# Kernel optimization log

Measured on AMD Instinct MI355X. Metric: run time of the kernel, lower is better.

Reference implementation:

```python
import jax, jax.numpy as jnp
import numpy as np

B, N, C, H, FF = 8, 1024, 256, 8, 4
HD = C // H

def _lin(key, din, dout):
    kw, kb = jax.random.split(key)
    lim = 1.0 / np.sqrt(din)
    W = jax.random.uniform(kw, (din, dout), minval=-lim, maxval=lim, dtype=jnp.float32)
    b = jax.random.uniform(kb, (dout,), minval=-lim, maxval=lim, dtype=jnp.float32)
    return W, b

def setup_inputs():
    key = jax.random.key(0)
    k = jax.random.split(key, 8)
    h = jax.random.normal(k[0], (B, N, C), dtype=jnp.float32)
    coords = jax.random.normal(k[1], (B, N, 3), dtype=jnp.float32) * 3.0
    mask = jnp.broadcast_to(jnp.arange(N) < int(0.9 * N), (B, N))
    Wq, bq = _lin(k[2], C, C)
    Wk, bk = _lin(k[3], C, C)
    Wv, bv = _lin(k[4], C, C)
    Wo, bo = _lin(k[5], C, C)
    Wf1, bf1 = _lin(k[6], C, FF * C)
    Wf2, bf2 = _lin(k[7], FF * C, C)
    g1 = jnp.ones((C,), jnp.float32); b1 = jnp.zeros((C,), jnp.float32)
    g2 = jnp.ones((C,), jnp.float32); b2 = jnp.zeros((C,), jnp.float32)
    return dict(h=h, coords=coords, mask=mask, Wq=Wq, bq=bq, Wk=Wk, bk=bk,
                Wv=Wv, bv=bv, Wo=Wo, bo=bo, g1=g1, b1=b1, g2=g2, b2=b2,
                Wf1=Wf1, bf1=bf1, Wf2=Wf2, bf2=bf2)

def _layernorm(x, g, b, eps=1e-5):
    mu = x.mean(-1, keepdims=True)
    var = ((x - mu) ** 2).mean(-1, keepdims=True)
    return (x - mu) / jnp.sqrt(var + eps) * g + b

def _forward(h, coords, mask, Wq, bq, Wk, bk, Wv, bv, Wo, bo,
             g1, b1, g2, b2, Wf1, bf1, Wf2, bf2):
    B_, N_, C_ = h.shape
    scale = HD ** (-0.5)
    eps = 1e-8
    # pairwise squared distance, +inf for pairs touching a masked node
    pair_mask = mask[:, :, None] & mask[:, None, :]          # [B,N,N]
    diff = coords[:, :, None, :] - coords[:, None, :, :]      # [B,N,N,3]
    r2 = jnp.where(pair_mask, (diff * diff).sum(-1), jnp.inf)
    eye = jnp.eye(N_, dtype=bool)[None]                       # [1,N,N]
    valid = jnp.isfinite(r2)
    off = valid & ~eye
    r2_off = jnp.where(off, r2, 0.0)
    cnt_row = jnp.maximum(off.sum(-1, keepdims=True), 1)
    r2_row_mean = jnp.maximum(r2_off.sum(-1, keepdims=True) / cnt_row, 1e-4)
    r2_eff = jnp.where(eye, r2_row_mean, r2)
    r2_eff = jnp.clip(jnp.nan_to_num(r2_eff, posinf=1e8), 1e-6, 1e8)
    w_raw = jnp.where(valid, 1.0 / (r2_eff + eps), 0.0)
    w = w_raw / jnp.maximum(w_raw.sum(-1, keepdims=True), 1e-12)
    log_w = jnp.log(jnp.maximum(w, 1e-12))[:, None]           # [B,1,N,N]
    # attention
    x = _layernorm(h, g1, b1)
    q = (x @ Wq + bq).reshape(B_, N_, H, HD).transpose(0, 2, 1, 3)
    k = (x @ Wk + bk).reshape(B_, N_, H, HD).transpose(0, 2, 1, 3)
    v = (x @ Wv + bv).reshape(B_, N_, H, HD).transpose(0, 2, 1, 3)
    logits = jnp.einsum('bhnd,bhmd->bhnm', q, k) * scale + log_w
    mask_q = mask[:, None, :, None]
    mask_k = mask[:, None, None, :]
    pair_valid = valid[:, None] & mask_q & mask_k
    logits = jnp.where(pair_valid, logits, -1e9)
    logits = jnp.where(mask_q, logits, 0.0)
    attn = jax.nn.softmax(logits, axis=-1)
    attn = jnp.nan_to_num(attn, nan=0.0)
    out = jnp.einsum('bhnm,bhmd->bhnd', attn, v)
    out = out * mask_q.astype(out.dtype)
    out = out.transpose(0, 2, 1, 3).reshape(B_, N_, C_)
    out = out @ Wo + bo
    h = h + out
    y = _layernorm(h, g2, b2)
    y = jax.nn.gelu(y @ Wf1 + bf1, approximate=False) @ Wf2 + bf2
    return h + y

def reference(h, coords, mask, Wq, bq, Wk, bk, Wv, bv, Wo, bo,
              g1, b1, g2, b2, Wf1, bf1, Wf2, bf2):
    return _forward(h, coords, mask, Wq, bq, Wk, bk, Wv, bv, Wo, bo,
                    g1, b1, g2, b2, Wf1, bf1, Wf2, bf2)
```

## Files before the change

### kernel.cpp

```cpp
#include <hip/hip_runtime.h>
#include <math.h>

#define NN 1024
#define CC 256
#define HH 8
#define HDD 32
#define NV 921
#define WJ 960

typedef __bf16 bf16x8 __attribute__((ext_vector_type(8)));
typedef float f32x4 __attribute__((ext_vector_type(4)));
typedef float f32x16 __attribute__((ext_vector_type(16)));
typedef unsigned short u16x4 __attribute__((ext_vector_type(4)));
typedef unsigned short u16x8 __attribute__((ext_vector_type(8)));
typedef unsigned int u32x4 __attribute__((ext_vector_type(4)));

static __device__ __forceinline__ unsigned short f2b(float x) {
  union { __bf16 h; unsigned short u; } c; c.h = (__bf16)x; return c.u;
}
static __device__ __forceinline__ float b2f(unsigned short u) {
  union { float f; unsigned v; } c; c.v = ((unsigned)u) << 16; return c.f;
}

static __device__ __forceinline__ unsigned cvt_pk_bf16(float lo, float hi) {
  unsigned r;
  asm("v_cvt_pk_bf16_f32 %0, %1, %2" : "=v"(r) : "v"(lo), "v"(hi));
  return r;
}

static __device__ __forceinline__ float block_sum(float val, float* red) {
  #pragma unroll
  for (int off = 32; off > 0; off >>= 1) val += __shfl_xor(val, off);
  __syncthreads();
  if ((threadIdx.x & 63) == 0) red[threadIdx.x >> 6] = val;
  __syncthreads();
  return red[0] + red[1] + red[2] + red[3];
}

__global__ __launch_bounds__(256) void prep_kernel(
    const float* __restrict__ coords, unsigned short* __restrict__ wP,
    const float* __restrict__ Wq, const float* __restrict__ Wk, const float* __restrict__ Wv,
    const float* __restrict__ Wo, const float* __restrict__ Wf1, const float* __restrict__ Wf2,
    unsigned short* __restrict__ qkvT, unsigned short* __restrict__ woT,
    unsigned short* __restrict__ wf1T, unsigned short* __restrict__ wf2T,
    const float* __restrict__ bq, const float* __restrict__ bk, const float* __restrict__ bv,
    float* __restrict__ bqkv,
    const float* __restrict__ h, const float* __restrict__ g1, const float* __restrict__ b1,
    unsigned short* __restrict__ x1b)
{
  __shared__ float smem[NN * 3 + 4];
  int bid = blockIdx.x;
  int tid = threadIdx.x;

  if (bid < 8192) {
    float* csh = smem;
    float* red = smem + NN * 3;
    int row = bid;
    int b = row >> 10, i = row & (NN - 1);
    unsigned short* wrow = wP + (size_t)row * WJ;
    if (i >= NV) {
      if (tid < 240) {
        ushort4 z = {0, 0, 0, 0};
        *(ushort4*)(wrow + tid * 4) = z;
      }
      return;
    }
    const float* cb = coords + (size_t)b * NN * 3;
    for (int t = tid; t < NN * 3; t += 256) csh[t] = cb[t];
    __syncthreads();
    float cix = csh[i*3+0], ciy = csh[i*3+1], ciz = csh[i*3+2];
    float r2loc[4];
    float part = 0.f;
    #pragma unroll
    for (int it = 0; it < 4; it++) {
      int j = tid + it * 256;
      float dx = cix - csh[j*3+0], dy = ciy - csh[j*3+1], dz = ciz - csh[j*3+2];
      float r2 = dx*dx + dy*dy + dz*dz;
      r2loc[it] = r2;
      if (j < NV && j != i) part += r2;
    }
    float s = block_sum(part, red);
    float rm = fmaxf(s * (1.0f / 920.0f), 1e-4f);
    float wpart = 0.f;
    #pragma unroll
    for (int it = 0; it < 4; it++) {
      int j = tid + it * 256;
      if (j < NV) {
        float r2e = (j == i) ? rm : r2loc[it];
        float r2c = fminf(fmaxf(r2e, 1e-6f), 1e8f);
        wpart += 1.0f / (r2c + 1e-8f);
      }
    }
    float sw = block_sum(wpart, red);
    float invsw = 1.0f / fmaxf(sw, 1e-12f);
    if (tid < 240) {
      ushort4 o;
      unsigned short* op = (unsigned short*)&o;
      #pragma unroll
      for (int e = 0; e < 4; e++) {
        int j = tid * 4 + e;
        float wv = 0.f;
        if (j < NV) {
          float dx = cix - csh[j*3+0], dy = ciy - csh[j*3+1], dz = ciz - csh[j*3+2];
          float r2 = dx*dx + dy*dy + dz*dz;
          float r2e = (j == i) ? rm : r2;
          float r2c = fminf(fmaxf(r2e, 1e-6f), 1e8f);
          wv = fmaxf((1.0f / (r2c + 1e-8f)) * invsw, 1e-12f);
        }
        op[e] = f2b(wv);
      }
      *(ushort4*)(wrow + tid * 4) = o;
    }
  } else if (bid < 8961) {
    int t = bid - 8192;
    if (t == 768) {
      bqkv[tid] = bq[tid]; bqkv[256 + tid] = bk[tid]; bqkv[512 + tid] = bv[tid];
      return;
    }
    float (*lds)[33] = (float(*)[33])smem;
    const float* src; unsigned short* dst; int Kd, Nd, tk, tn;
    if (t < 256) {
      int wid = t >> 6, lt = t & 63;
      const float* srcs[4] = {Wq, Wk, Wv, Wo};
      unsigned short* dsts[4] = {qkvT, qkvT + 256 * 256, qkvT + 512 * 256, woT};
      src = srcs[wid]; dst = dsts[wid]; Kd = 256; Nd = 256; tk = lt >> 3; tn = lt & 7;
    } else if (t < 512) {
      int lt = t - 256;
      src = Wf1; dst = wf1T; Kd = 256; Nd = 1024; tk = lt >> 5; tn = lt & 31;
    } else {
      int lt = t - 512;
      src = Wf2; dst = wf2T; Kd = 1024; Nd = 256; tk = lt >> 3; tn = lt & 7;
    }
    int tx = tid & 31, ty = tid >> 5;
    #pragma unroll
    for (int it = 0; it < 4; it++) {
      int r = ty + it * 8;
      lds[r][tx] = src[(size_t)(tk * 32 + r) * Nd + tn * 32 + tx];
    }
    __syncthreads();
    #pragma unroll
    for (int it = 0; it < 4; it++) {
      int r = ty + it * 8;
      dst[(size_t)(tn * 32 + r) * Kd + tk * 32 + tx] = f2b(lds[tx][r]);
    }
  } else {
    int w = tid >> 6, lane = tid & 63;
    int row = (bid - 8961) * 4 + w;
    float4 x = *(const float4*)(h + (size_t)row * CC + lane * 4);
    float s = x.x + x.y + x.z + x.w;
    #pragma unroll
    for (int off = 1; off < 64; off <<= 1) s += __shfl_xor(s, off);
    float mu = s * (1.0f / 256.0f);
    float dx0 = x.x - mu, dx1 = x.y - mu, dx2 = x.z - mu, dx3 = x.w - mu;
    float s2 = dx0*dx0 + dx1*dx1 + dx2*dx2 + dx3*dx3;
    #pragma unroll
    for (int off = 1; off < 64; off <<= 1) s2 += __shfl_xor(s2, off);
    float rstd = 1.0f / sqrtf(s2 * (1.0f / 256.0f) + 1e-5f);
    float4 gv = *(const float4*)(g1 + lane * 4);
    float4 bv2 = *(const float4*)(b1 + lane * 4);
    ushort4 o;
    o.x = f2b(dx0 * rstd * gv.x + bv2.x);
    o.y = f2b(dx1 * rstd * gv.y + bv2.y);
    o.z = f2b(dx2 * rstd * gv.z + bv2.z);
    o.w = f2b(dx3 * rstd * gv.w + bv2.w);
    *(ushort4*)(x1b + (size_t)row * CC + lane * 4) = o;
  }
}

__global__ __launch_bounds__(256) void ln_bf16_kernel(
    const float* __restrict__ X, const float* __restrict__ g, const float* __restrict__ b,
    unsigned short* __restrict__ out)
{
  int w = threadIdx.x >> 6, lane = threadIdx.x & 63;
  int row = blockIdx.x * 4 + w;
  float4 x = *(const float4*)(X + (size_t)row * CC + lane * 4);
  float s = x.x + x.y + x.z + x.w;
  #pragma unroll
  for (int off = 1; off < 64; off <<= 1) s += __shfl_xor(s, off);
  float mu = s * (1.0f / 256.0f);
  float dx0 = x.x - mu, dx1 = x.y - mu, dx2 = x.z - mu, dx3 = x.w - mu;
  float s2 = dx0*dx0 + dx1*dx1 + dx2*dx2 + dx3*dx3;
  #pragma unroll
  for (int off = 1; off < 64; off <<= 1) s2 += __shfl_xor(s2, off);
  float rstd = 1.0f / sqrtf(s2 * (1.0f / 256.0f) + 1e-5f);
  float4 gv = *(const float4*)(g + lane * 4);
  float4 bv = *(const float4*)(b + lane * 4);
  ushort4 o;
  o.x = f2b(dx0 * rstd * gv.x + bv.x);
  o.y = f2b(dx1 * rstd * gv.y + bv.y);
  o.z = f2b(dx2 * rstd * gv.z + bv.z);
  o.w = f2b(dx3 * rstd * gv.w + bv.w);
  *(ushort4*)(out + (size_t)row * CC + lane * 4) = o;
}

template<bool GELU_EP, bool RES_ADD, int OUT_MODE>
__global__ __launch_bounds__(256) void gemm_mfma_kernel(
    const unsigned short* __restrict__ A, const unsigned short* __restrict__ BT,
    const float* __restrict__ bias, const float* __restrict__ res,
    void* __restrict__ out, float oscale, int M, int N, int K)
{
  __shared__ unsigned short As[128][72];
  __shared__ unsigned short Bs[64][72];
  int tid = threadIdx.x;
  int w = tid >> 6, lane = tid & 63, lo = lane & 15, hi = lane >> 4;
  int wr = w >> 1, wc = w & 1;
  int bm = blockIdx.y * 128, bn = blockIdx.x * 64;
  f32x4 acc[4][2];
  #pragma unroll
  for (int a = 0; a < 4; a++)
    #pragma unroll
    for (int nf = 0; nf < 2; nf++) acc[a][nf] = (f32x4){0.f, 0.f, 0.f, 0.f};
  int arow = tid >> 3, acol = (tid & 7) * 8;
  u16x8 areg[4], breg[2];
  #pragma unroll
  for (int it = 0; it < 4; it++)
    areg[it] = *(const u16x8*)(A + (size_t)(bm + arow + it * 32) * K + acol);
  #pragma unroll
  for (int it = 0; it < 2; it++)
    breg[it] = *(const u16x8*)(BT + (size_t)(bn + arow + it * 32) * K + acol);
  for (int k0 = 0; k0 < K; k0 += 64) {
    __syncthreads();
    #pragma unroll
    for (int it = 0; it < 4; it++) *(u16x8*)&As[arow + it * 32][acol] = areg[it];
    #pragma unroll
    for (int it = 0; it < 2; it++) *(u16x8*)&Bs[arow + it * 32][acol] = breg[it];
    __syncthreads();
    if (k0 + 64 < K) {
      #pragma unroll
      for (int it = 0; it < 4; it++)
        areg[it] = *(const u16x8*)(A + (size_t)(bm + arow + it * 32) * K + k0 + 64 + acol);
      #pragma unroll
      for (int it = 0; it < 2; it++)
        breg[it] = *(const u16x8*)(BT + (size_t)(bn + arow + it * 32) * K + k0 + 64 + acol);
    }
    #pragma unroll
    for (int ks = 0; ks < 2; ks++) {
      bf16x8 bf0 = *(const bf16x8*)&Bs[wc * 32 + lo][ks * 32 + hi * 8];
      bf16x8 bf1 = *(const bf16x8*)&Bs[wc * 32 + 16 + lo][ks * 32 + hi * 8];
      #pragma unroll
      for (int a = 0; a < 4; a++) {
        bf16x8 af = *(const bf16x8*)&As[wr * 64 + a * 16 + lo][ks * 32 + hi * 8];
        acc[a][0] = __builtin_amdgcn_mfma_f32_16x16x32_bf16(af, bf0, acc[a][0], 0, 0, 0);
        acc[a][1] = __builtin_amdgcn_mfma_f32_16x16x32_bf16(af, bf1, acc[a][1], 0, 0, 0);
      }
    }
  }
  float bias0 = bias[bn + wc * 32 + lo];
  float bias1 = bias[bn + wc * 32 + 16 + lo];
  #pragma unroll
  for (int a = 0; a < 4; a++) {
    int gm0 = bm + wr * 64 + a * 16 + hi * 4;
    #pragma unroll
    for (int nf = 0; nf < 2; nf++) {
      int gn = bn + wc * 32 + nf * 16 + lo;
      float bb = nf ? bias1 : bias0;
      float vv[4];
      #pragma unroll
      for (int r = 0; r < 4; r++) {
        float v = acc[a][nf][r] + bb;
        if constexpr (RES_ADD) v += res[(size_t)(gm0 + r) * N + gn];
        if constexpr (GELU_EP) v = 0.5f * v * (1.0f + erff(v * 0.70710678118654752f));
        vv[r] = v;
      }
      if constexpr (OUT_MODE == 0) {
        float* of = (float*)out;
        #pragma unroll
        for (int r = 0; r < 4; r++) of[(size_t)(gm0 + r) * N + gn] = vv[r] * oscale;
      } else if constexpr (OUT_MODE == 1) {
        unsigned short* ob = (unsigned short*)out;
        #pragma unroll
        for (int r = 0; r < 4; r++) ob[(size_t)(gm0 + r) * N + gn] = f2b(vv[r] * oscale);
      } else {
        int cb = gn >> 8;
        int nl = gn & 255;
        unsigned short* qp = (unsigned short*)out;
        if (cb == 0) {
          #pragma unroll
          for (int r = 0; r < 4; r++) qp[(size_t)(gm0 + r) * 256 + nl] = f2b(vv[r] * oscale);
        } else if (cb == 1) {
          unsigned short* kp = qp + (size_t)M * 256;
          #pragma unroll
          for (int r = 0; r < 4; r++) kp[(size_t)(gm0 + r) * 256 + nl] = f2b(vv[r]);
        } else {
          unsigned short* vp = qp + (size_t)M * 512;
          int bidx = gm0 >> 10, tok = gm0 & 1023;
          ushort4 pk;
          pk.x = f2b(vv[0]); pk.y = f2b(vv[1]); pk.z = f2b(vv[2]); pk.w = f2b(vv[3]);
          *(ushort4*)&vp[(((size_t)(bidx * 256 + nl)) << 10) + tok] = pk;
        }
      }
    }
  }
}

__global__ __launch_bounds__(256, 2) void attn_mfma_kernel(
    const __bf16* __restrict__ q, const __bf16* __restrict__ k, const __bf16* __restrict__ vt,
    const unsigned short* __restrict__ wP, unsigned short* __restrict__ ao)
{
  __shared__ unsigned short Ktu[64][136];
  __shared__ unsigned short VTs[128][72];
  __shared__ unsigned short Wls[32][68];

  int tid = threadIdx.x;
  int w = tid >> 6;
  int lane = tid & 63;
  int il = lane & 31, hf = lane >> 5;
  int b = blockIdx.z, hg = blockIdx.y, it = blockIdx.x;
  int i0 = it * 32;
  int head = hg * 4 + w;
  int ig = i0 + il;

  const __bf16* qrow = q + ((size_t)(b * NN + ig)) * CC + head * HDD;
  bf16x8 qf0 = *(const bf16x8*)(qrow + hf * 8);
  bf16x8 qf1 = *(const bf16x8*)(qrow + 16 + hf * 8);

  f32x16 osum;
  #pragma unroll
  for (int r = 0; r < 16; r++) osum[r] = 0.f;
  float den = 0.f;

  int sjr = tid >> 4, scpos = (tid & 15) * 8;
  int vrow = tid >> 1, vcol = (tid & 1) * 32;
  int wrow = tid >> 3, wcol = (tid & 7) * 8;

  u16x8 kreg[4], vreg[4], wreg;

  if (i0 < NV) {
    {
      const __bf16* ksrc = k + ((size_t)(b * NN + sjr)) * CC + hg * 128 + scpos;
      #pragma unroll
      for (int rr = 0; rr < 4; rr++)
        kreg[rr] = *(const u16x8*)(ksrc + (size_t)(rr * 16) * CC);
      const __bf16* vsrc = vt + ((size_t)(b * CC + hg * 128 + vrow)) * NN + vcol;
      #pragma unroll
      for (int qq = 0; qq < 4; qq++)
        vreg[qq] = *(const u16x8*)(vsrc + qq * 8);
      wreg = *(const u16x8*)(wP + ((size_t)(b * NN + i0 + wrow)) * WJ + wcol);
    }
    for (int jt = 0; jt < 15; jt++) {
      __syncthreads();
      #pragma unroll
      for (int rr = 0; rr < 4; rr++)
        *(u16x8*)&Ktu[sjr + rr * 16][scpos] = kreg[rr];
      #pragma unroll
      for (int qq = 0; qq < 4; qq++)
        *(u16x8*)&VTs[vrow][vcol + qq * 8] = vreg[qq];
      *(u16x8*)&Wls[wrow][wcol] = wreg;
      __syncthreads();
      if (jt < 14) {
        int j0 = (jt + 1) * 64;
        const __bf16* ksrc = k + ((size_t)(b * NN + j0 + sjr)) * CC + hg * 128 + scpos;
        #pragma unroll
        for (int rr = 0; rr < 4; rr++)
          kreg[rr] = *(const u16x8*)(ksrc + (size_t)(rr * 16) * CC);
        const __bf16* vsrc = vt + ((size_t)(b * CC + hg * 128 + vrow)) * NN + j0 + vcol;
        #pragma unroll
        for (int qq = 0; qq < 4; qq++)
          vreg[qq] = *(const u16x8*)(vsrc + qq * 8);
        wreg = *(const u16x8*)(wP + ((size_t)(b * NN + i0 + wrow)) * WJ + j0 + wcol);
      }

      #pragma unroll
      for (int jblk = 0; jblk < 2; jblk++) {
        f32x16 s;
        #pragma unroll
        for (int r = 0; r < 16; r++) s[r] = 0.f;
        bf16x8 kf0 = *(const bf16x8*)&Ktu[jblk * 32 + il][w * 32 + hf * 8];
        bf16x8 kf1 = *(const bf16x8*)&Ktu[jblk * 32 + il][w * 32 + 16 + hf * 8];
        s = __builtin_amdgcn_mfma_f32_32x32x16_bf16(kf0, qf0, s, 0, 0, 0);
        s = __builtin_amdgcn_mfma_f32_32x32x16_bf16(kf1, qf1, s, 0, 0, 0);
        float p[16];
        #pragma unroll
        for (int qd = 0; qd < 4; qd++) {
          u16x4 w4 = *(const u16x4*)&Wls[il][jblk * 32 + qd * 8 + hf * 4];
          #pragma unroll
          for (int e = 0; e < 4; e++) {
            int r = qd * 4 + e;
            float pv = b2f(w4[e]) * __expf(s[r]);
            den += pv;
            p[r] = pv;
          }
        }
        #pragma unroll
        for (int kw = 0; kw < 2; kw++) {
          unsigned pk0 = cvt_pk_bf16(p[8 * kw + 0], p[8 * kw + 1]);
          unsigned pk1 = cvt_pk_bf16(p[8 * kw + 2], p[8 * kw + 3]);
          unsigned pk2 = cvt_pk_bf16(p[8 * kw + 4], p[8 * kw + 5]);
          unsigned pk3 = cvt_pk_bf16(p[8 * kw + 6], p[8 * kw + 7]);
          u32x4 frag;
#if __has_builtin(__builtin_amdgcn_permlane32_swap)
          {
            typedef unsigned uint2v __attribute__((ext_vector_type(2)));
            uint2v s02 = __builtin_amdgcn_permlane32_swap(pk0, pk2, false, false);
            uint2v s13 = __builtin_amdgcn_permlane32_swap(pk1, pk3, false, false);
            frag[0] = s02[0]; frag[1] = s13[0]; frag[2] = s02[1]; frag[3] = s13[1];
          }
#else
          {
            unsigned t0 = __shfl_xor((int)pk2, 32);
            unsigned t1 = __shfl_xor((int)pk3, 32);
            unsigned t2 = __shfl_xor((int)pk0, 32);
            unsigned t3 = __shfl_xor((int)pk1, 32);
            frag[0] = hf ? t0 : pk0;
            frag[1] = hf ? t1 : pk1;
            frag[2] = hf ? pk2 : t2;
            frag[3] = hf ? pk3 : t3;
          }
#endif
          bf16x8 pfrag;
          { union { u32x4 u; bf16x8 b; } cvt; cvt.u = frag; pfrag = cvt.b; }
          bf16x8 vfrag = *(const bf16x8*)&VTs[w * 32 + il][(jblk * 2 + kw) * 16 + hf * 8];
          osum = __builtin_amdgcn_mfma_f32_32x32x16_bf16(pfrag, vfrag, osum, 0, 0, 0);
        }
      }
    }
  }

  den += __shfl_xor(den, 32);
  float inv = (den > 0.f) ? 1.0f / den : 0.f;

  #pragma unroll
  for (int r = 0; r < 16; r++) {
    int ir = (r & 3) + 8 * (r >> 2) + 4 * hf;
    float sc = __shfl(inv, ir);
    ao[((size_t)(b * NN + i0 + ir)) * CC + head * HDD + il] = f2b(osum[r] * sc);
  }
}

extern "C" void kernel_launch(void* const* d_in, const int* in_sizes, int n_in,
                              void* d_out, int out_size, void* d_ws, size_t ws_size,
                              hipStream_t stream) {
  (void)in_sizes; (void)n_in; (void)out_size; (void)ws_size;
  const float* h      = (const float*)d_in[0];
  const float* coords = (const float*)d_in[1];
  const float* Wq  = (const float*)d_in[3];
  const float* bq  = (const float*)d_in[4];
  const float* Wk  = (const float*)d_in[5];
  const float* bk  = (const float*)d_in[6];
  const float* Wv  = (const float*)d_in[7];
  const float* bv  = (const float*)d_in[8];
  const float* Wo  = (const float*)d_in[9];
  const float* bo  = (const float*)d_in[10];
  const float* g1  = (const float*)d_in[11];
  const float* b1  = (const float*)d_in[12];
  const float* g2  = (const float*)d_in[13];
  const float* b2  = (const float*)d_in[14];
  const float* Wf1 = (const float*)d_in[15];
  const float* bf1 = (const float*)d_in[16];
  const float* Wf2 = (const float*)d_in[17];
  const float* bf2 = (const float*)d_in[18];

  const int M = 8 * NN;
  char* cur = (char*)d_ws;
  auto alloc = [&](size_t bytes) { char* p = cur; cur += (bytes + 255) & ~(size_t)255; return p; };
  unsigned short* wPb  = (unsigned short*)alloc((size_t)M * WJ * 2);
  unsigned short* qkvT = (unsigned short*)alloc(768 * 256 * 2);
  unsigned short* woT  = (unsigned short*)alloc(256 * 256 * 2);
  unsigned short* wf1T = (unsigned short*)alloc(1024 * 256 * 2);
  unsigned short* wf2T = (unsigned short*)alloc(256 * 1024 * 2);
  float* bqkv = (float*)alloc(768 * 4);
  unsigned short* x1b = (unsigned short*)alloc((size_t)M * CC * 2);
  unsigned short* x2b = (unsigned short*)alloc((size_t)M * CC * 2);
  unsigned short* qb  = (unsigned short*)alloc((size_t)M * CC * 2);
  unsigned short* kb_ = (unsigned short*)alloc((size_t)M * CC * 2);
  unsigned short* vtb = (unsigned short*)alloc((size_t)M * CC * 2);
  unsigned short* aob = (unsigned short*)alloc((size_t)M * CC * 2);
  unsigned short* y1b = qb;
  float* h1 = (float*)d_out;

  const float QSCALE = 0.17677669529663687f;

  prep_kernel<<<11009, 256, 0, stream>>>(
      coords, wPb, Wq, Wk, Wv, Wo, Wf1, Wf2,
      qkvT, woT, wf1T, wf2T, bq, bk, bv, bqkv, h, g1, b1, x1b);

  gemm_mfma_kernel<false, false, 3><<<dim3(12, 64), 256, 0, stream>>>(
      x1b, qkvT, bqkv, nullptr, qb, QSCALE, M, 768, 256);

  attn_mfma_kernel<<<dim3(32, 2, 8), 256, 0, stream>>>(
      (const __bf16*)qb, (const __bf16*)kb_, (const __bf16*)vtb, wPb, aob);

  gemm_mfma_kernel<false, true, 0><<<dim3(4, 64), 256, 0, stream>>>(
      aob, woT, bo, h, h1, 1.0f, M, 256, 256);

  ln_bf16_kernel<<<M / 4, 256, 0, stream>>>(h1, g2, b2, x2b);

  gemm_mfma_kernel<true, false, 1><<<dim3(16, 64), 256, 0, stream>>>(
      x2b, wf1T, bf1, nullptr, y1b, 1.0f, M, 1024, 256);

  gemm_mfma_kernel<false, true, 0><<<dim3(4, 64), 256, 0, stream>>>(
      y1b, wf2T, bf2, h1, d_out, 1.0f, M, 256, 1024);
}
```

Measured before the change: 105.1 us.

## Batch four weight rows per prep block, template GEMM tile height, use exp2 softmax

The prep kernel now handles four rows of the distance-weight matrix per block, so each block loads the coordinate tile into shared memory once for four rows and the launch needs fewer blocks. The GEMM kernel takes its M tile height as a template parameter, and the two N=256 GEMMs switch to 64-row tiles to double their grid size and fill more compute units. The attention softmax uses exp2 with the log2(e) factor folded into the query scale, which removes a multiply per logit. The trade-offs are a less parallel prep phase with extra block barriers per row, and smaller tiles that give up some operand reuse in the GEMMs.

```diff
diff --git a/kernel.cpp b/kernel.cpp
--- a/kernel.cpp
+++ b/kernel.cpp
@@ -52,67 +52,73 @@
   int bid = blockIdx.x;
   int tid = threadIdx.x;
 
-  if (bid < 8192) {
+  if (bid < 2048) {
     float* csh = smem;
     float* red = smem + NN * 3;
-    int row = bid;
-    int b = row >> 10, i = row & (NN - 1);
-    unsigned short* wrow = wP + (size_t)row * WJ;
-    if (i >= NV) {
-      if (tid < 240) {
-        ushort4 z = {0, 0, 0, 0};
-        *(ushort4*)(wrow + tid * 4) = z;
-      }
-      return;
-    }
+    int base = bid * 4;
+    int b = base >> 10;
     const float* cb = coords + (size_t)b * NN * 3;
     for (int t = tid; t < NN * 3; t += 256) csh[t] = cb[t];
     __syncthreads();
-    float cix = csh[i*3+0], ciy = csh[i*3+1], ciz = csh[i*3+2];
-    float r2loc[4];
-    float part = 0.f;
-    #pragma unroll
-    for (int it = 0; it < 4; it++) {
-      int j = tid + it * 256;
-      float dx = cix - csh[j*3+0], dy = ciy - csh[j*3+1], dz = ciz - csh[j*3+2];
-      float r2 = dx*dx + dy*dy + dz*dz;
-      r2loc[it] = r2;
-      if (j < NV && j != i) part += r2;
-    }
-    float s = block_sum(part, red);
-    float rm = fmaxf(s * (1.0f / 920.0f), 1e-4f);
-    float wpart = 0.f;
-    #pragma unroll
-    for (int it = 0; it < 4; it++) {
-      int j = tid + it * 256;
-      if (j < NV) {
-        float r2e = (j == i) ? rm : r2loc[it];
-        float r2c = fminf(fmaxf(r2e, 1e-6f), 1e8f);
-        wpart += 1.0f / (r2c + 1e-8f);
-      }
-    }
-    float sw = block_sum(wpart, red);
-    float invsw = 1.0f / fmaxf(sw, 1e-12f);
-    if (tid < 240) {
-      ushort4 o;
-      unsigned short* op = (unsigned short*)&o;
-      #pragma unroll
-      for (int e = 0; e < 4; e++) {
-        int j = tid * 4 + e;
-        float wv = 0.f;
+    #pragma unroll
+    for (int ii = 0; ii < 4; ii++) {
+      int row = base + ii;
+      int i = row & (NN - 1);
+      unsigned short* wrow = wP + (size_t)row * WJ;
+      if (i >= NV) {
+        if (tid < 240) {
+          ushort4 z = {0, 0, 0, 0};
+          *(ushort4*)(wrow + tid * 4) = z;
+        }
+        continue;
+      }
+      float cix = csh[i*3+0], ciy = csh[i*3+1], ciz = csh[i*3+2];
+      float r2loc[4];
+      float part = 0.f;
+      #pragma unroll
+      for (int it = 0; it < 4; it++) {
+        int j = tid + it * 256;
+        float dx = cix - csh[j*3+0], dy = ciy - csh[j*3+1], dz = ciz - csh[j*3+2];
+        float r2 = dx*dx + dy*dy + dz*dz;
+        r2loc[it] = r2;
+        if (j < NV && j != i) part += r2;
+      }
+      float s = block_sum(part, red);
+      float rm = fmaxf(s * (1.0f / 920.0f), 1e-4f);
+      float wpart = 0.f;
+      #pragma unroll
+      for (int it = 0; it < 4; it++) {
+        int j = tid + it * 256;
         if (j < NV) {
-          float dx = cix - csh[j*3+0], dy = ciy - csh[j*3+1], dz = ciz - csh[j*3+2];
-          float r2 = dx*dx + dy*dy + dz*dz;
-          float r2e = (j == i) ? rm : r2;
+          float r2e = (j == i) ? rm : r2loc[it];
           float r2c = fminf(fmaxf(r2e, 1e-6f), 1e8f);
-          wv = fmaxf((1.0f / (r2c + 1e-8f)) * invsw, 1e-12f);
+          wpart += 1.0f / (r2c + 1e-8f);
         }
-        op[e] = f2b(wv);
-      }
-      *(ushort4*)(wrow + tid * 4) = o;
-    }
-  } else if (bid < 8961) {
-    int t = bid - 8192;
+      }
+      float sw = block_sum(wpart, red);
+      float invsw = 1.0f / fmaxf(sw, 1e-12f);
+      if (tid < 240) {
+        ushort4 o;
+        unsigned short* op = (unsigned short*)&o;
+        #pragma unroll
+        for (int e = 0; e < 4; e++) {
+          int j = tid * 4 + e;
+          float wv = 0.f;
+          if (j < NV) {
+            float dx = cix - csh[j*3+0], dy = ciy - csh[j*3+1], dz = ciz - csh[j*3+2];
+            float r2 = dx*dx + dy*dy + dz*dz;
+            float r2e = (j == i) ? rm : r2;
+            float r2c = fminf(fmaxf(r2e, 1e-6f), 1e8f);
+            wv = fmaxf((1.0f / (r2c + 1e-8f)) * invsw, 1e-12f);
+          }
+          op[e] = f2b(wv);
+        }
+        *(ushort4*)(wrow + tid * 4) = o;
+      }
+      __syncthreads();
+    }
+  } else if (bid < 2817) {
+    int t = bid - 2048;
     if (t == 768) {
       bqkv[tid] = bq[tid]; bqkv[256 + tid] = bk[tid]; bqkv[512 + tid] = bv[tid];
       return;
@@ -145,7 +151,7 @@
     }
   } else {
     int w = tid >> 6, lane = tid & 63;
-    int row = (bid - 8961) * 4 + w;
+    int row = (bid - 2817) * 4 + w;
     float4 x = *(const float4*)(h + (size_t)row * CC + lane * 4);
     float s = x.x + x.y + x.z + x.w;
     #pragma unroll
@@ -193,27 +199,28 @@
   *(ushort4*)(out + (size_t)row * CC + lane * 4) = o;
 }
 
-template<bool GELU_EP, bool RES_ADD, int OUT_MODE>
+template<int BM, bool GELU_EP, bool RES_ADD, int OUT_MODE>
 __global__ __launch_bounds__(256) void gemm_mfma_kernel(
     const unsigned short* __restrict__ A, const unsigned short* __restrict__ BT,
     const float* __restrict__ bias, const float* __restrict__ res,
     void* __restrict__ out, float oscale, int M, int N, int K)
 {
-  __shared__ unsigned short As[128][72];
+  constexpr int AFRAG = BM / 32;
+  __shared__ unsigned short As[BM][72];
   __shared__ unsigned short Bs[64][72];
   int tid = threadIdx.x;
   int w = tid >> 6, lane = tid & 63, lo = lane & 15, hi = lane >> 4;
   int wr = w >> 1, wc = w & 1;
-  int bm = blockIdx.y * 128, bn = blockIdx.x * 64;
-  f32x4 acc[4][2];
-  #pragma unroll
-  for (int a = 0; a < 4; a++)
+  int bm = blockIdx.y * BM, bn = blockIdx.x * 64;
+  f32x4 acc[AFRAG][2];
+  #pragma unroll
+  for (int a = 0; a < AFRAG; a++)
     #pragma unroll
     for (int nf = 0; nf < 2; nf++) acc[a][nf] = (f32x4){0.f, 0.f, 0.f, 0.f};
   int arow = tid >> 3, acol = (tid & 7) * 8;
-  u16x8 areg[4], breg[2];
-  #pragma unroll
-  for (int it = 0; it < 4; it++)
+  u16x8 areg[AFRAG], breg[2];
+  #pragma unroll
+  for (int it = 0; it < AFRAG; it++)
     areg[it] = *(const u16x8*)(A + (size_t)(bm + arow + it * 32) * K + acol);
   #pragma unroll
   for (int it = 0; it < 2; it++)
@@ -221,13 +228,13 @@
   for (int k0 = 0; k0 < K; k0 += 64) {
     __syncthreads();
     #pragma unroll
-    for (int it = 0; it < 4; it++) *(u16x8*)&As[arow + it * 32][acol] = areg[it];
+    for (int it = 0; it < AFRAG; it++) *(u16x8*)&As[arow + it * 32][acol] = areg[it];
     #pragma unroll
     for (int it = 0; it < 2; it++) *(u16x8*)&Bs[arow + it * 32][acol] = breg[it];
     __syncthreads();
     if (k0 + 64 < K) {
       #pragma unroll
-      for (int it = 0; it < 4; it++)
+      for (int it = 0; it < AFRAG; it++)
         areg[it] = *(const u16x8*)(A + (size_t)(bm + arow + it * 32) * K + k0 + 64 + acol);
       #pragma unroll
       for (int it = 0; it < 2; it++)
@@ -238,8 +245,8 @@
       bf16x8 bf0 = *(const bf16x8*)&Bs[wc * 32 + lo][ks * 32 + hi * 8];
       bf16x8 bf1 = *(const bf16x8*)&Bs[wc * 32 + 16 + lo][ks * 32 + hi * 8];
       #pragma unroll
-      for (int a = 0; a < 4; a++) {
-        bf16x8 af = *(const bf16x8*)&As[wr * 64 + a * 16 + lo][ks * 32 + hi * 8];
+      for (int a = 0; a < AFRAG; a++) {
+        bf16x8 af = *(const bf16x8*)&As[wr * (BM / 2) + a * 16 + lo][ks * 32 + hi * 8];
         acc[a][0] = __builtin_amdgcn_mfma_f32_16x16x32_bf16(af, bf0, acc[a][0], 0, 0, 0);
         acc[a][1] = __builtin_amdgcn_mfma_f32_16x16x32_bf16(af, bf1, acc[a][1], 0, 0, 0);
       }
@@ -248,8 +255,8 @@
   float bias0 = bias[bn + wc * 32 + lo];
   float bias1 = bias[bn + wc * 32 + 16 + lo];
   #pragma unroll
-  for (int a = 0; a < 4; a++) {
-    int gm0 = bm + wr * 64 + a * 16 + hi * 4;
+  for (int a = 0; a < AFRAG; a++) {
+    int gm0 = bm + wr * (BM / 2) + a * 16 + hi * 4;
     #pragma unroll
     for (int nf = 0; nf < 2; nf++) {
       int gn = bn + wc * 32 + nf * 16 + lo;
@@ -376,7 +383,7 @@
           #pragma unroll
           for (int e = 0; e < 4; e++) {
             int r = qd * 4 + e;
-            float pv = b2f(w4[e]) * __expf(s[r]);
+            float pv = b2f(w4[e]) * __builtin_exp2f(s[r]);
             den += pv;
             p[r] = pv;
           }
@@ -468,26 +475,26 @@
   unsigned short* y1b = qb;
   float* h1 = (float*)d_out;
 
-  const float QSCALE = 0.17677669529663687f;
-
-  prep_kernel<<<11009, 256, 0, stream>>>(
+  const float QSCALE2 = 0.25503486904512874f;
+
+  prep_kernel<<<4865, 256, 0, stream>>>(
       coords, wPb, Wq, Wk, Wv, Wo, Wf1, Wf2,
       qkvT, woT, wf1T, wf2T, bq, bk, bv, bqkv, h, g1, b1, x1b);
 
-  gemm_mfma_kernel<false, false, 3><<<dim3(12, 64), 256, 0, stream>>>(
-      x1b, qkvT, bqkv, nullptr, qb, QSCALE, M, 768, 256);
+  gemm_mfma_kernel<128, false, false, 3><<<dim3(12, 64), 256, 0, stream>>>(
+      x1b, qkvT, bqkv, nullptr, qb, QSCALE2, M, 768, 256);
 
   attn_mfma_kernel<<<dim3(32, 2, 8), 256, 0, stream>>>(
       (const __bf16*)qb, (const __bf16*)kb_, (const __bf16*)vtb, wPb, aob);
 
-  gemm_mfma_kernel<false, true, 0><<<dim3(4, 64), 256, 0, stream>>>(
+  gemm_mfma_kernel<64, false, true, 0><<<dim3(4, 128), 256, 0, stream>>>(
       aob, woT, bo, h, h1, 1.0f, M, 256, 256);
 
   ln_bf16_kernel<<<M / 4, 256, 0, stream>>>(h1, g2, b2, x2b);
 
-  gemm_mfma_kernel<true, false, 1><<<dim3(16, 64), 256, 0, stream>>>(
+  gemm_mfma_kernel<128, true, false, 1><<<dim3(16, 64), 256, 0, stream>>>(
       x2b, wf1T, bf1, nullptr, y1b, 1.0f, M, 1024, 256);
 
-  gemm_mfma_kernel<false, true, 0><<<dim3(4, 64), 256, 0, stream>>>(
+  gemm_mfma_kernel<64, false, true, 0><<<dim3(4, 128), 256, 0, stream>>>(
       y1b, wf2T, bf2, h1, d_out, 1.0f, M, 256, 1024);
 }
```

Measured after the change: 107.1 us. About the same (+1.9%).
